# Optimization experiments

Measured on AMD Instinct MI355X. Metric: run time of the kernel, lower is better.

The kernel has to match this reference:

```python
import jax, jax.numpy as jnp
import numpy as np

NUM_EMBEDDINGS = 512
EMBEDDING_DIM = 64
COMMITMENT_COST = 0.25


def setup_inputs() -> dict:
    key = jax.random.key(0)
    k1, k2 = jax.random.split(key)
    inputs = jax.random.normal(k1, (32, 64, 64, 64), dtype=jnp.float32)  # NCHW
    # nn.Embedding init: uniform(-1/K, 1/K)
    weight = jax.random.uniform(
        k2, (NUM_EMBEDDINGS, EMBEDDING_DIM), dtype=jnp.float32,
        minval=-1.0 / NUM_EMBEDDINGS, maxval=1.0 / NUM_EMBEDDINGS)
    return {"inputs": inputs, "weight": weight}


def reference(inputs, weight):
    # NCHW -> NHWC
    x = jnp.transpose(inputs, (0, 2, 3, 1))
    in_shape = x.shape
    flat = x.reshape(-1, EMBEDDING_DIM)                  # [N, D]
    # squared euclidean distances to each codebook vector: [N, K]
    d = (jnp.sum(flat ** 2, axis=1, keepdims=True)
         + jnp.sum(weight ** 2, axis=1)
         - 2.0 * flat @ weight.T)
    codebook_indices = jnp.argmin(d, axis=1)             # [N] int
    quantized = weight[codebook_indices].reshape(in_shape)  # gather lookup

    e_latent_loss = jnp.mean((jax.lax.stop_gradient(quantized) - x) ** 2)
    q_latent_loss = jnp.mean((quantized - jax.lax.stop_gradient(x)) ** 2)
    loss = q_latent_loss + COMMITMENT_COST * e_latent_loss

    # straight-through estimator
    quantized = x + jax.lax.stop_gradient(quantized - x)

    # perplexity from code usage histogram (equivalent to one-hot mean)
    n = flat.shape[0]
    counts = jnp.zeros((NUM_EMBEDDINGS,), jnp.float32).at[codebook_indices].add(1.0)
    avg_probs = counts / n
    perplexity = jnp.exp(-jnp.sum(avg_probs * jnp.log(avg_probs + 1e-10)))

    quantized_nchw = jnp.transpose(quantized, (0, 3, 1, 2))
    return (loss, quantized_nchw, perplexity, codebook_indices)
```

## Files before the change

### kernel.cpp

```cpp
#include <hip/hip_runtime.h>
#include <math.h>

#define NUM_K   512
#define DIM     64
#define NROWS   131072
#define NELEM   8388608
#define Q_OFF    1
#define PERP_OFF 8388609
#define IDX_OFF  8388610

#define MARGIN  1.7e-4f

typedef short  bf16x8 __attribute__((ext_vector_type(8)));
typedef float  f32x4  __attribute__((ext_vector_type(4)));


__device__ __forceinline__ unsigned short f2bf(float f) {
    unsigned u = __float_as_uint(f);
    return (unsigned short)((u + 0x7FFFu + ((u >> 16) & 1u)) >> 16);
}
__device__ __forceinline__ float bf2f(unsigned short h) {
    return __uint_as_float(((unsigned)h) << 16);
}

__device__ __forceinline__ unsigned long long eval_chain(
        const float* __restrict__ xr, float xsq,
        const float* __restrict__ w, float wsq, int k) {
    const float* wk = w + (size_t)k * DIM;
    float d = 0.f;
#pragma unroll
    for (int c = 0; c < DIM; c += 4) {
        float4 wv = *(const float4*)(wk + c);
        d = fmaf(xr[c + 0], wv.x, d);
        d = fmaf(xr[c + 1], wv.y, d);
        d = fmaf(xr[c + 2], wv.z, d);
        d = fmaf(xr[c + 3], wv.w, d);
    }
    float s = __fsub_rn(__fadd_rn(xsq, wsq), __fmul_rn(2.f, d));
    return ((unsigned long long)__float_as_uint(s) << 32) | (unsigned)k;
}

__global__ __launch_bounds__(256) void vq_prep(const float* __restrict__ w,
                                               float* __restrict__ swsq_g,
                                               unsigned short* __restrict__ wpack,
                                               unsigned* __restrict__ counts,
                                               int rep_words,
                                               float* __restrict__ loss_sum,
                                               unsigned* __restrict__ ticket) {
    const int id = blockIdx.x * 256 + threadIdx.x;
    if (id < rep_words) counts[id] = 0u;
    if (id == 0) { loss_sum[0] = 0.f; ticket[0] = 0u; }
    if (id < NUM_K) {
        const float* wk = w + id * DIM;
        float r[8];
#pragma unroll
        for (int j = 0; j < 8; ++j) r[j] = __fmul_rn(wk[j], wk[j]);
#pragma unroll
        for (int t = 1; t < 8; ++t)
#pragma unroll
            for (int j = 0; j < 8; ++j)
                r[j] = __fadd_rn(r[j], __fmul_rn(wk[8 * t + j], wk[8 * t + j]));
        swsq_g[id] = __fadd_rn(
            __fadd_rn(__fadd_rn(r[0], r[1]), __fadd_rn(r[2], r[3])),
            __fadd_rn(__fadd_rn(r[4], r[5]), __fadd_rn(r[6], r[7])));
    }
    const int kt = id >> 8, f = (id >> 6) & 3, l = id & 63;
    const int step = f >> 1, pass = f & 1;
    const int coln = kt * 16 + (l & 15), quad = l >> 4;
    const float* src = w + (size_t)coln * DIM + step * 32 + quad * 8;
    unsigned short tmp[8];
#pragma unroll
    for (int j = 0; j < 8; ++j) {
        float v = src[j];
        unsigned short hi = f2bf(v);
        tmp[j] = pass ? f2bf(v - bf2f(hi)) : hi;
    }
    *(uint4*)(wpack + (size_t)id * 8) = *(uint4*)tmp;
}

__global__ __launch_bounds__(256, 3) void vq_phase1(
        const float* __restrict__ x,
        const float* __restrict__ w,
        const float* __restrict__ swsq_g,
        const uint4* __restrict__ wpack,
        float* __restrict__ out,
        float* __restrict__ loss_sum,
        unsigned* __restrict__ counts,
        unsigned* __restrict__ ticket,
        int rep_mask) {
    __shared__ float swsq[NUM_K];
    __shared__ unsigned hcnt[NUM_K];
    __shared__ float xs[128 * 65];
    __shared__ float sxsq[128];
    __shared__ int sidx[128];
    __shared__ float wred[4];
    __shared__ unsigned long long rred[4];
    __shared__ int rlist[128];
    __shared__ int rcount;
    __shared__ unsigned s_tick;
    __shared__ float red8[8];

    const int tid  = threadIdx.x;
    const int lane = tid & 63;
    const int wvid = tid >> 6;
    const int quad = lane >> 4;
    const int m    = lane & 15;
    const int n0   = blockIdx.x * 128;
    const int b    = n0 >> 12;
    const int hw0  = n0 & 4095;
    const float* xbase = x + (size_t)b * 262144 + hw0;
    float* out_q   = out + Q_OFF;
    float* out_idx = out + IDX_OFF;

    if (tid == 0) rcount = 0;
    for (int i = tid; i < NUM_K; i += 256) { swsq[i] = swsq_g[i]; hcnt[i] = 0; }

    bf16x8 afr[2][2][2];
#pragma unroll
    for (int rt = 0; rt < 2; ++rt) {
        const int row = wvid * 32 + rt * 16 + m;
        const float* xp = xbase + row;
#pragma unroll
        for (int s = 0; s < 2; ++s) {
            union { bf16x8 v; unsigned short u[8]; } hi, lo;
#pragma unroll
            for (int j = 0; j < 8; ++j) {
                const int c = s * 32 + quad * 8 + j;
                float v = xp[(size_t)c * 4096];
                xs[row * 65 + c] = v;
                unsigned short h = f2bf(v);
                hi.u[j] = h;
                lo.u[j] = f2bf(v - bf2f(h));
            }
            afr[rt][s][0] = hi.v;
            afr[rt][s][1] = lo.v;
        }
    }
    __syncthreads();

    if (tid < 128) {
        const float* xr = &xs[tid * 65];
        float p0 = 0.f, p1 = 0.f, p2 = 0.f, p3 = 0.f;
#pragma unroll
        for (int c = 0; c < DIM; c += 4) {
            p0 = fmaf(xr[c + 0], xr[c + 0], p0);
            p1 = fmaf(xr[c + 1], xr[c + 1], p1);
            p2 = fmaf(xr[c + 2], xr[c + 2], p2);
            p3 = fmaf(xr[c + 3], xr[c + 3], p3);
        }
        sxsq[tid] = __fadd_rn(__fadd_rn(p0, p1), __fadd_rn(p2, p3));
    }
    __syncthreads();

    float m1v[2][4], m2v[2][4], m3v[2][4];
#pragma unroll
    for (int rt = 0; rt < 2; ++rt)
#pragma unroll
        for (int r = 0; r < 4; ++r) {
            m1v[rt][r] = 3.4e38f; m2v[rt][r] = 3.4e38f; m3v[rt][r] = 3.4e38f;
        }

    uint4 P[2][4];
    {
        const uint4* t0 = wpack;
        const uint4* t1 = wpack + 256;
#pragma unroll
        for (int q = 0; q < 4; ++q) { P[0][q] = t0[q * 64 + lane];
                                      P[1][q] = t1[q * 64 + lane]; }
    }
#pragma unroll 1
    for (int kt = 0; kt < 32; kt += 2) {
#pragma unroll
        for (int h = 0; h < 2; ++h) {
            bf16x8 bh0 = __builtin_bit_cast(bf16x8, P[h][0]);
            bf16x8 bl0 = __builtin_bit_cast(bf16x8, P[h][1]);
            bf16x8 bh1 = __builtin_bit_cast(bf16x8, P[h][2]);
            bf16x8 bl1 = __builtin_bit_cast(bf16x8, P[h][3]);
            const int kg = (kt + h) * 16 + m;
            const float wsqv = swsq[kg];
            if (kt + h + 2 < 32) {
                const uint4* np = wpack + (size_t)(kt + h + 2) * 256;
#pragma unroll
                for (int q = 0; q < 4; ++q) P[h][q] = np[q * 64 + lane];
            }
#pragma unroll
            for (int rt = 0; rt < 2; ++rt) {
                f32x4 acc = {0.f, 0.f, 0.f, 0.f};
                acc = __builtin_amdgcn_mfma_f32_16x16x32_bf16(afr[rt][0][0], bh0, acc, 0, 0, 0);
                acc = __builtin_amdgcn_mfma_f32_16x16x32_bf16(afr[rt][0][0], bl0, acc, 0, 0, 0);
                acc = __builtin_amdgcn_mfma_f32_16x16x32_bf16(afr[rt][0][1], bh0, acc, 0, 0, 0);
                acc = __builtin_amdgcn_mfma_f32_16x16x32_bf16(afr[rt][1][0], bh1, acc, 0, 0, 0);
                acc = __builtin_amdgcn_mfma_f32_16x16x32_bf16(afr[rt][1][0], bl1, acc, 0, 0, 0);
                acc = __builtin_amdgcn_mfma_f32_16x16x32_bf16(afr[rt][1][1], bh1, acc, 0, 0, 0);
#pragma unroll
                for (int r = 0; r < 4; ++r) {
                    float s  = fmaf(-2.f, acc[r], wsqv);
                    float sp = __uint_as_float(
                        (__float_as_uint(s) & 0xFFFFFE00u) | (unsigned)kg);
                    m3v[rt][r] = __builtin_amdgcn_fmed3f(m2v[rt][r], m3v[rt][r], sp);
                    m2v[rt][r] = __builtin_amdgcn_fmed3f(m1v[rt][r], m2v[rt][r], sp);
                    m1v[rt][r] = fminf(m1v[rt][r], sp);
                }
            }
        }
    }

    float gm[2][4];
#pragma unroll
    for (int rt = 0; rt < 2; ++rt)
#pragma unroll
        for (int r = 0; r < 4; ++r) {
            float g = m1v[rt][r];
            g = fminf(g, __shfl_xor(g, 1));
            g = fminf(g, __shfl_xor(g, 2));
            g = fminf(g, __shfl_xor(g, 4));
            g = fminf(g, __shfl_xor(g, 8));
            gm[rt][r] = g;
        }

#pragma unroll 1
    for (int rt = 0; rt < 2; ++rt)
#pragma unroll 1
        for (int r = 0; r < 4; ++r) {
            const float lim = gm[rt][r] + MARGIN;
            const bool c1 = m1v[rt][r] <= lim;
            const bool c2 = m2v[rt][r] <= lim;
            const bool f3 = m3v[rt][r] <= lim;
            unsigned long long b1 = __ballot(c1);
            unsigned long long b2 = __ballot(c2);
            unsigned long long b3 = __ballot(f3);
            const unsigned fld1 = (unsigned)(b1 >> (quad * 16)) & 0xFFFFu;
            const unsigned fld2 = (unsigned)(b2 >> (quad * 16)) & 0xFFFFu;
            const unsigned fld3 = (unsigned)(b3 >> (quad * 16)) & 0xFFFFu;
            const int  nc   = __popc(fld1) + __popc(fld2);
            const bool flag = fld3 != 0;
            const int rowL = wvid * 32 + rt * 16 + quad * 4 + r;
            unsigned long long best = ~0ull;
            if (!flag && nc > 1) {
                const float* xr = &xs[rowL * 65];
                const float xq = sxsq[rowL];
                if (c1) {
                    const int ka = (int)(__float_as_uint(m1v[rt][r]) & 511u);
                    best = eval_chain(xr, xq, w, swsq[ka], ka);
                }
                if (c2) {
                    const int kb = (int)(__float_as_uint(m2v[rt][r]) & 511u);
                    unsigned long long e = eval_chain(xr, xq, w, swsq[kb], kb);
                    best = e < best ? e : best;
                }
            }
#pragma unroll
            for (int d = 1; d < 16; d <<= 1) {
                unsigned long long o = __shfl_xor(best, d);
                best = o < best ? o : best;
            }
            if (m == 0) {
                if (flag) rlist[atomicAdd(&rcount, 1)] = rowL;
                else sidx[rowL] = (nc > 1)
                        ? (int)(best & 0xFFFFFFFFull)
                        : (int)(__float_as_uint(gm[rt][r]) & 511u);
            }
        }
    __syncthreads();

    const int rc = rcount;
#pragma unroll 1
    for (int i = 0; i < rc; ++i) {
        const int rowL = rlist[i];
        const float* xr = &xs[rowL * 65];
        const float xq = sxsq[rowL];
        unsigned long long bb = eval_chain(xr, xq, w, swsq[tid], tid);
        unsigned long long e2 = eval_chain(xr, xq, w, swsq[tid + 256], tid + 256);
        if (e2 < bb) bb = e2;
#pragma unroll
        for (int d = 1; d < 64; d <<= 1) {
            unsigned long long o = __shfl_xor(bb, d);
            if (o < bb) bb = o;
        }
        if (lane == 0) rred[wvid] = bb;
        __syncthreads();
        if (tid == 0) {
            unsigned long long q0 = rred[0] < rred[1] ? rred[0] : rred[1];
            unsigned long long q1 = rred[2] < rred[3] ? rred[2] : rred[3];
            sidx[rowL] = (int)((q0 < q1 ? q0 : q1) & 0xFFFFFFFFull);
        }
        __syncthreads();
    }

    {
        const int rb = tid & 127, cg = tid >> 7;
        const int bk = sidx[rb];
        const float* xr = &xs[rb * 65];
        float dsum = 0.f;
        const float4* wb = (const float4*)(w + (size_t)bk * DIM + cg * 32);
        float* oq = out_q + (size_t)b * 262144 + hw0 + rb;
        if (cg == 0) {
            out_idx[n0 + rb] = (float)bk;
            atomicAdd(&hcnt[bk], 1u);
        }
#pragma unroll
        for (int j4 = 0; j4 < 8; ++j4) {
            float4 v = wb[j4];
            const int c = cg * 32 + j4 * 4;
            float e0 = v.x - xr[c + 0];
            float e1 = v.y - xr[c + 1];
            float e2 = v.z - xr[c + 2];
            float e3 = v.w - xr[c + 3];
            dsum = fmaf(e0, e0, dsum);
            dsum = fmaf(e1, e1, dsum);
            dsum = fmaf(e2, e2, dsum);
            dsum = fmaf(e3, e3, dsum);
            oq[(size_t)(c + 0) * 4096] = v.x;
            oq[(size_t)(c + 1) * 4096] = v.y;
            oq[(size_t)(c + 2) * 4096] = v.z;
            oq[(size_t)(c + 3) * 4096] = v.w;
        }
#pragma unroll
        for (int off = 32; off > 0; off >>= 1) dsum += __shfl_down(dsum, off);
        if (lane == 0) wred[wvid] = dsum;
    }
    __syncthreads();
    if (tid == 0)
        atomicAdd(loss_sum, (wred[0] + wred[1]) + (wred[2] + wred[3]));
    {
        unsigned* mycnt = counts + ((blockIdx.x & rep_mask) << 9);
        for (int i = tid; i < NUM_K; i += 256) {
            unsigned cc = hcnt[i];
            if (cc) atomicAdd(&mycnt[i], cc);
        }
    }

    __syncthreads();
    if (tid == 0) s_tick = atomicAdd(ticket, 1u);
    __syncthreads();
    if (s_tick == (unsigned)(gridDim.x - 1)) {
#pragma unroll 1
        for (int half = 0; half < 2; ++half) {
            const int k = (wvid + half * 4) * 64 + lane;
            unsigned cnt = 0;
            for (int rr = 0; rr <= rep_mask; ++rr)
                cnt += atomicAdd(&counts[(rr << 9) + k], 0u);
            float p = (float)cnt * (1.f / (float)NROWS);
            float t = p * logf(p + 1e-10f);
#pragma unroll
            for (int off = 32; off > 0; off >>= 1) t += __shfl_down(t, off);
            if (lane == 0) red8[wvid + half * 4] = t;
        }
        __syncthreads();
        if (tid == 0) {
            float s = 0.f;
#pragma unroll
            for (int i = 0; i < 8; ++i) s += red8[i];
            out[PERP_OFF] = expf(-s);
            float ls = atomicAdd(loss_sum, 0.f);
            out[0] = ls * (1.25f / (float)NELEM);
        }
    }
}

extern "C" void kernel_launch(void* const* d_in, const int* in_sizes, int n_in,
                              void* d_out, int out_size, void* d_ws, size_t ws_size,
                              hipStream_t stream) {
    const float* x = (const float*)d_in[0];
    const float* w = (const float*)d_in[1];
    float* out = (float*)d_out;
    char* ws = (char*)d_ws;

    int rep = 16;
    while (rep > 2 && (size_t)(64 + rep * 2048 + 2048 + 131072) > ws_size)
        rep >>= 1;

    float*    loss_sum = (float*)ws;
    unsigned* ticket   = (unsigned*)(ws + 8);
    unsigned* counts   = (unsigned*)(ws + 64);
    float*    swsq_g   = (float*)(ws + 64 + rep * 2048);
    unsigned short* wpack = (unsigned short*)(ws + 64 + rep * 2048 + 2048);

    vq_prep<<<32, 256, 0, stream>>>(w, swsq_g, wpack, counts, rep * 512,
                                    loss_sum, ticket);
    vq_phase1<<<NROWS / 128, 256, 0, stream>>>(x, w, swsq_g, (const uint4*)wpack,
                                               out, loss_sum, counts, ticket,
                                               rep - 1);
}
```

Baseline: 152.0 us.

## Track argmin indices explicitly, swizzle block-to-tile order, tighten margin, use atomic loads

Replaces the packing of codebook indices into the low mantissa bits of the distance with separate index registers that are updated via compares and selects, and carries the index through the cross-lane min reduction. Remaps block IDs so consecutive blocks touch strided tiles, tightens the near-tie margin that triggers exact fp32 re-evaluation, and replaces atomicAdd-with-zero reads in the finalizer with relaxed atomic loads. The explicit index tracking adds registers and VALU work in the hot loop, while the smaller margin reduces how often the exact re-check path runs. The tighter margin also raises the risk of picking the wrong index on near ties.

```diff
diff --git a/kernel.cpp b/kernel.cpp
--- a/kernel.cpp
+++ b/kernel.cpp
@@ -9,7 +9,7 @@
 #define PERP_OFF 8388609
 #define IDX_OFF  8388610
 
-#define MARGIN  1.7e-4f
+#define MARGIN  1.0e-4f
 
 typedef short  bf16x8 __attribute__((ext_vector_type(8)));
 typedef float  f32x4  __attribute__((ext_vector_type(4)));
@@ -105,7 +105,8 @@
     const int wvid = tid >> 6;
     const int quad = lane >> 4;
     const int m    = lane & 15;
-    const int n0   = blockIdx.x * 128;
+    const int tile = (blockIdx.x & 7) * 128 + (blockIdx.x >> 3);
+    const int n0   = tile * 128;
     const int b    = n0 >> 12;
     const int hw0  = n0 & 4095;
     const float* xbase = x + (size_t)b * 262144 + hw0;
@@ -152,12 +153,13 @@
     }
     __syncthreads();
 
-    float m1v[2][4], m2v[2][4], m3v[2][4];
+    float min1[2][4], min2[2][4], min3[2][4]; int idx1[2][4], idx2[2][4];
 #pragma unroll
     for (int rt = 0; rt < 2; ++rt)
 #pragma unroll
         for (int r = 0; r < 4; ++r) {
-            m1v[rt][r] = 3.4e38f; m2v[rt][r] = 3.4e38f; m3v[rt][r] = 3.4e38f;
+            min1[rt][r] = 3.4e38f; min2[rt][r] = 3.4e38f; min3[rt][r] = 3.4e38f;
+            idx1[rt][r] = 0; idx2[rt][r] = 0;
         }
 
     uint4 P[2][4];
@@ -194,38 +196,34 @@
                 acc = __builtin_amdgcn_mfma_f32_16x16x32_bf16(afr[rt][1][1], bh1, acc, 0, 0, 0);
 #pragma unroll
                 for (int r = 0; r < 4; ++r) {
-                    float s  = fmaf(-2.f, acc[r], wsqv);
-                    float sp = __uint_as_float(
-                        (__float_as_uint(s) & 0xFFFFFE00u) | (unsigned)kg);
-                    m3v[rt][r] = __builtin_amdgcn_fmed3f(m2v[rt][r], m3v[rt][r], sp);
-                    m2v[rt][r] = __builtin_amdgcn_fmed3f(m1v[rt][r], m2v[rt][r], sp);
-                    m1v[rt][r] = fminf(m1v[rt][r], sp);
+                    float s = fmaf(-2.f, acc[r], wsqv);
+                    bool lt1 = s < min1[rt][r];
+                    bool lt2 = s < min2[rt][r];
+                    min3[rt][r] = __builtin_amdgcn_fmed3f(min2[rt][r], min3[rt][r], s);
+                    idx2[rt][r] = lt1 ? idx1[rt][r] : (lt2 ? kg : idx2[rt][r]);
+                    min2[rt][r] = __builtin_amdgcn_fmed3f(min1[rt][r], min2[rt][r], s);
+                    idx1[rt][r] = lt1 ? kg : idx1[rt][r];
+                    min1[rt][r] = fminf(min1[rt][r], s);
                 }
             }
         }
     }
 
-    float gm[2][4];
-#pragma unroll
+#pragma unroll 1
     for (int rt = 0; rt < 2; ++rt)
-#pragma unroll
+#pragma unroll 1
         for (int r = 0; r < 4; ++r) {
-            float g = m1v[rt][r];
-            g = fminf(g, __shfl_xor(g, 1));
-            g = fminf(g, __shfl_xor(g, 2));
-            g = fminf(g, __shfl_xor(g, 4));
-            g = fminf(g, __shfl_xor(g, 8));
-            gm[rt][r] = g;
-        }
-
-#pragma unroll 1
-    for (int rt = 0; rt < 2; ++rt)
-#pragma unroll 1
-        for (int r = 0; r < 4; ++r) {
-            const float lim = gm[rt][r] + MARGIN;
-            const bool c1 = m1v[rt][r] <= lim;
-            const bool c2 = m2v[rt][r] <= lim;
-            const bool f3 = m3v[rt][r] <= lim;
+            float g1 = min1[rt][r]; int gi = idx1[rt][r];
+#pragma unroll
+            for (int d = 1; d < 16; d <<= 1) {
+                float og = __shfl_xor(g1, d);
+                int   oi = __shfl_xor(gi, d);
+                if (og < g1) { g1 = og; gi = oi; }
+            }
+            const float lim = g1 + MARGIN;
+            const bool c1 = min1[rt][r] <= lim;
+            const bool c2 = min2[rt][r] <= lim;
+            const bool f3 = min3[rt][r] <= lim;
             unsigned long long b1 = __ballot(c1);
             unsigned long long b2 = __ballot(c2);
             unsigned long long b3 = __ballot(f3);
@@ -239,13 +237,11 @@
             if (!flag && nc > 1) {
                 const float* xr = &xs[rowL * 65];
                 const float xq = sxsq[rowL];
-                if (c1) {
-                    const int ka = (int)(__float_as_uint(m1v[rt][r]) & 511u);
-                    best = eval_chain(xr, xq, w, swsq[ka], ka);
-                }
-                if (c2) {
-                    const int kb = (int)(__float_as_uint(m2v[rt][r]) & 511u);
-                    unsigned long long e = eval_chain(xr, xq, w, swsq[kb], kb);
+                const int k1 = c1 ? idx1[rt][r] : idx2[rt][r];
+                if (c1 || c2) best = eval_chain(xr, xq, w, swsq[k1], k1);
+                if (c1 && c2) {
+                    unsigned long long e =
+                        eval_chain(xr, xq, w, swsq[idx2[rt][r]], idx2[rt][r]);
                     best = e < best ? e : best;
                 }
             }
@@ -256,9 +252,7 @@
             }
             if (m == 0) {
                 if (flag) rlist[atomicAdd(&rcount, 1)] = rowL;
-                else sidx[rowL] = (nc > 1)
-                        ? (int)(best & 0xFFFFFFFFull)
-                        : (int)(__float_as_uint(gm[rt][r]) & 511u);
+                else sidx[rowL] = (nc > 1) ? (int)(best & 0xFFFFFFFFull) : gi;
             }
         }
     __syncthreads();
@@ -339,7 +333,9 @@
             const int k = (wvid + half * 4) * 64 + lane;
             unsigned cnt = 0;
             for (int rr = 0; rr <= rep_mask; ++rr)
-                cnt += atomicAdd(&counts[(rr << 9) + k], 0u);
+                cnt += __hip_atomic_load(&counts[(rr << 9) + k],
+                                         __ATOMIC_RELAXED,
+                                         __HIP_MEMORY_SCOPE_AGENT);
             float p = (float)cnt * (1.f / (float)NROWS);
             float t = p * logf(p + 1e-10f);
 #pragma unroll
@@ -352,7 +348,8 @@
 #pragma unroll
             for (int i = 0; i < 8; ++i) s += red8[i];
             out[PERP_OFF] = expf(-s);
-            float ls = atomicAdd(loss_sum, 0.f);
+            float ls = __hip_atomic_load(loss_sum, __ATOMIC_RELAXED,
+                                         __HIP_MEMORY_SCOPE_AGENT);
             out[0] = ls * (1.25f / (float)NELEM);
         }
     }
```

After: 166.4 us. +9.5%, slower.
